# Performance work log

Measured on AMD Instinct MI355X. Metric: run time of the kernel, lower is better.

## Reference

```python
import jax, jax.numpy as jnp
import numpy as np


def setup_inputs() -> dict:
    key = jax.random.key(0)
    k0, k1, k2, k3 = jax.random.split(key, 4)
    B, in_dim, n_vars, out_dim, E = 64, 512, 512, 720, 8
    x = jax.random.normal(k0, (B, in_dim, n_vars), dtype=jnp.float32)
    # Gating: nn.Linear(in_dim, E, bias=False) -> weight [E, in_dim]
    Wg = jax.random.normal(k1, (E, in_dim), dtype=jnp.float32) * 0.02
    # Experts: nn.Linear(in_dim, out_dim) -> weight [out_dim, in_dim], bias [out_dim]
    We = jax.random.normal(k2, (E, out_dim, in_dim), dtype=jnp.float32) * 0.02
    be = jax.random.normal(k3, (E, out_dim), dtype=jnp.float32) * 0.02
    return {"x": x, "Wg": Wg, "We": We, "be": be, "top_k": 2}


def reference(x, Wg, We, be, top_k):
    # x: [B, in_len, n_vars] -> tokens along n_vars with feature dim in_len
    xt = jnp.swapaxes(x, 1, 2)                      # [B, V, D]
    gate = jax.nn.softmax(xt @ Wg.T, axis=-1)       # [B, V, E]
    weights, sel = jax.lax.top_k(gate, top_k)       # [B, V, k]
    E, O, D = We.shape
    out = jnp.zeros(xt.shape[:2] + (O,), dtype=xt.dtype)  # [B, V, O]
    for e in range(E):
        # combine weight for expert e: sum over top-k slots routed to e
        coef = jnp.sum(jnp.where(sel == e, weights, jnp.zeros_like(weights)), axis=-1)  # [B, V]
        out = out + coef[..., None] * (jnp.einsum('bvd,od->bvo', xt, We[e]) + be[e])
    return jnp.swapaxes(out, 1, 2)                  # [B, pred_len, n_vars]
```

## Files before the change

kernel.cpp:

```cpp
#include <hip/hip_runtime.h>
#include <hip/hip_bf16.h>

#define DID 512
#define NV  512
#define NB  64
#define OD  720
#define OPAD 768
#define NE  8
#define NTOK (NB * NV)
#define MAXTILE 512

typedef short  bf16x8 __attribute__((ext_vector_type(8)));
typedef float  f32x4  __attribute__((ext_vector_type(4)));

#define XT_OFF    0u
#define WB_OFF    33554432u
#define PID_OFF   39845888u
#define C1D_OFF   39976960u
#define C2D_OFF   40108032u
#define TL_OFF    40239104u
#define CL1_OFF   40370176u
#define CL2_OFF   40501248u
#define BCNT_OFF  40632320u
#define BFILL_OFF 40632576u
#define BOFF_OFF  40632832u
#define TPID_OFF  40633088u
#define TT0_OFF   40635136u
#define TEND_OFF  40637184u
#define NT_OFF    40639232u
#define SCR_OFF   40639488u
#define SCR_END   87825408u

static __device__ __forceinline__ ushort f2bf(float f) {
  unsigned u = __float_as_uint(f);
  unsigned r = (u + 0x7fffu + ((u >> 16) & 1u)) >> 16;
  return (ushort)r;
}
static __device__ __forceinline__ float bf2f(ushort u) {
  return __uint_as_float(((unsigned)u) << 16);
}
static __device__ __forceinline__ void async16(const ushort* g, ushort* l) {
  __builtin_amdgcn_global_load_lds((__attribute__((address_space(1))) void*)(g),
                                   (__attribute__((address_space(3))) void*)(l),
                                   16, 0, 0);
}
static __device__ __forceinline__ int swz(int r) { return (r & 3) ^ ((r >> 2) & 1); }

__global__ __launch_bounds__(512) void k_gatet(const float* __restrict__ x,
                                               const float* __restrict__ Wg,
                                               ushort* __restrict__ xt,
                                               int* __restrict__ pairid,
                                               float* __restrict__ c1d,
                                               float* __restrict__ c2d,
                                               int* __restrict__ bcnt) {
  __shared__ float wg[NE * DID];
  __shared__ float part[8][64][NE + 1];
  __shared__ int cnt64[64];
  const int tid = threadIdx.x;
  for (int i = tid; i < NE * DID / 4; i += 512)
    ((float4*)wg)[i] = ((const float4*)Wg)[i];
  if (tid < 64) cnt64[tid] = 0;
  __syncthreads();

  const int b    = blockIdx.y;
  const int v0   = blockIdx.x * 64;
  const int w    = tid >> 6;
  const int lane = tid & 63;
  const int v    = v0 + lane;
  const int d0   = w * 64;
  const float* xp = x + ((size_t)b * DID + d0) * NV + v;
  ushort* xtp = xt + ((size_t)b * NV + v) * DID + d0;

  float acc[NE];
#pragma unroll
  for (int e = 0; e < NE; ++e) acc[e] = 0.f;

  for (int c = 0; c < 64; c += 8) {
    float xv[8];
#pragma unroll
    for (int u = 0; u < 8; ++u) xv[u] = xp[(size_t)(c + u) * NV];
#pragma unroll
    for (int e = 0; e < NE; ++e) {
      const float* wp = &wg[e * DID + d0 + c];
      float4 wa = *(const float4*)wp;
      float4 wb4 = *(const float4*)(wp + 4);
      acc[e] += xv[0] * wa.x + xv[1] * wa.y + xv[2] * wa.z + xv[3] * wa.w
              + xv[4] * wb4.x + xv[5] * wb4.y + xv[6] * wb4.z + xv[7] * wb4.w;
    }
    bf16x8 pk;
#pragma unroll
    for (int u = 0; u < 8; ++u) pk[u] = (short)f2bf(xv[u]);
    *(bf16x8*)(xtp + c) = pk;
  }

#pragma unroll
  for (int e = 0; e < NE; ++e) part[w][lane][e] = acc[e];
  __syncthreads();

  if (tid < 64) {
    float a[NE];
#pragma unroll
    for (int e = 0; e < NE; ++e) {
      float s = part[0][tid][e];
#pragma unroll
      for (int q = 1; q < 8; ++q) s += part[q][tid][e];
      a[e] = s;
    }
    float mx = a[0];
#pragma unroll
    for (int e = 1; e < NE; ++e) mx = fmaxf(mx, a[e]);
    float sum = 0.f;
#pragma unroll
    for (int e = 0; e < NE; ++e) { a[e] = __expf(a[e] - mx); sum += a[e]; }
    const float inv = 1.f / sum;

    int i1 = 0; float g1 = a[0];
#pragma unroll
    for (int e = 1; e < NE; ++e) if (a[e] > g1) { g1 = a[e]; i1 = e; }
    int i2 = -1; float g2 = -1.f;
#pragma unroll
    for (int e = 0; e < NE; ++e) if (e != i1 && a[e] > g2) { g2 = a[e]; i2 = e; }
    g1 *= inv; g2 *= inv;

    int ea, eb; float ca, cb;
    if (i1 < i2) { ea = i1; eb = i2; ca = g1; cb = g2; }
    else         { ea = i2; eb = i1; ca = g2; cb = g1; }
    const int pid = ea * 8 + eb;
    const int t = b * NV + v0 + tid;
    pairid[t] = pid; c1d[t] = ca; c2d[t] = cb;
    atomicAdd(&cnt64[pid], 1);
  }
  __syncthreads();
  if (tid < 64 && cnt64[tid]) atomicAdd(&bcnt[tid], cnt64[tid]);
}

__global__ __launch_bounds__(256) void k_wbconv(const float* __restrict__ We,
                                                ushort* __restrict__ wb) {
  const int e = blockIdx.y;
  const int i = blockIdx.x * 256 + threadIdx.x;
  const int o = i >> 9;
  ushort val = 0;
  if (o < OD) val = f2bf(We[(size_t)e * OD * DID + i]);
  wb[(size_t)e * OPAD * DID + i] = val;
}

__global__ void k_prefix(const int* __restrict__ bcnt, int* __restrict__ boffs,
                         int* __restrict__ tpid, int* __restrict__ tt0,
                         int* __restrict__ tend, int* __restrict__ ntp) {
  const int p = threadIdx.x;
  const int c = bcnt[p];
  int run = c;
#pragma unroll
  for (int s = 1; s < 64; s <<= 1) {
    int up = __shfl_up(run, s, 64);
    if (p >= s) run += up;
  }
  const int excl = run - c;
  boffs[p] = excl;
  const int ntiles = (c + 127) >> 7;
  int trun = ntiles;
#pragma unroll
  for (int s = 1; s < 64; s <<= 1) {
    int up = __shfl_up(trun, s, 64);
    if (p >= s) trun += up;
  }
  const int texcl = trun - ntiles;
  for (int i = 0; i < ntiles; ++i) {
    tpid[texcl + i] = p;
    tt0[texcl + i]  = excl + i * 128;
    tend[texcl + i] = excl + c;
  }
  if (p == 63) ntp[0] = texcl + ntiles;
}

__global__ __launch_bounds__(256) void k_scatter(const int* __restrict__ pairid,
                                                 const float* __restrict__ c1d,
                                                 const float* __restrict__ c2d,
                                                 const int* __restrict__ boffs,
                                                 int* __restrict__ bfill,
                                                 int* __restrict__ tlist,
                                                 float* __restrict__ cl1,
                                                 float* __restrict__ cl2) {
  __shared__ int cnt64[64], base64[64];
  const int tid = threadIdx.x;
  if (tid < 64) cnt64[tid] = 0;
  __syncthreads();
  const int t = blockIdx.x * 256 + tid;
  const int pid = pairid[t];
  const int p = atomicAdd(&cnt64[pid], 1);
  __syncthreads();
  if (tid < 64) base64[tid] = cnt64[tid] ? atomicAdd(&bfill[tid], cnt64[tid]) : 0;
  __syncthreads();
  const int slot = boffs[pid] + base64[pid] + p;
  tlist[slot] = t; cl1[slot] = c1d[t]; cl2[slot] = c2d[t];
}

__global__ __launch_bounds__(256, 2) void k_gemm(
    const ushort* __restrict__ xt, const ushort* __restrict__ wb,
    const float* __restrict__ be, const int* __restrict__ tlist,
    const float* __restrict__ cl1, const float* __restrict__ cl2,
    const int* __restrict__ tpid, const int* __restrict__ tt0,
    const int* __restrict__ tendarr, const int* __restrict__ ntp,
    ushort* __restrict__ scratch, float* __restrict__ out, int mode) {
  const int tile = blockIdx.x;
  if (tile >= ntp[0]) return;
  const int pid  = tpid[tile];
  const int t0   = tt0[tile];
  const int tend = tendarr[tile];
  const int e1 = pid >> 3, e2 = pid & 7;
  const int o0 = blockIdx.y * 256;

  __shared__ __align__(16) ushort As[3][8192];
  __shared__ __align__(16) ushort Bs[3][4096];

  const int tid  = threadIdx.x;
  const int lane = tid & 63;
  const int w    = tid >> 6;

  int aoffA[4];
#pragma unroll
  for (int i = 0; i < 4; ++i) {
    const int f = w * 256 + i * 64 + lane;
    const int r = f >> 2, p = f & 3, q = p ^ swz(r);
    aoffA[i] = (o0 + r) * DID + q * 8;
  }
  int boffB[2];
#pragma unroll
  for (int i = 0; i < 2; ++i) {
    const int f = w * 128 + i * 64 + lane;
    const int r = f >> 2, p = f & 3, q = p ^ swz(r);
    const int sl = t0 + r;
    const int tk = (sl < tend) ? tlist[sl] : 0;
    boffB[i] = tk * DID + q * 8;
  }

  const int m    = lane & 15;
  const int quad = lane >> 4;
  const int wt   = (w & 1) * 64;
  const int wo   = (w >> 1) * 128;

  float ratio[4], c2v[4]; int tokv[4]; bool gv[4];
#pragma unroll
  for (int j = 0; j < 4; ++j) {
    const int sl = t0 + wt + j * 16 + m;
    gv[j] = sl < tend;
    const float cc1 = gv[j] ? cl1[sl] : 0.f;
    const float cc2 = gv[j] ? cl2[sl] : 1.f;
    ratio[j] = cc1 / cc2;
    c2v[j]   = gv[j] ? cc2 : 0.f;
    tokv[j]  = gv[j] ? tlist[sl] : 0;
  }

  f32x4 acc[8][4];
#pragma unroll
  for (int i = 0; i < 8; ++i)
#pragma unroll
    for (int j = 0; j < 4; ++j) acc[i][j] = (f32x4){0.f, 0.f, 0.f, 0.f};

#define STAGE(t, buf) do {                                          \
    const int eA_ = ((t) < 16) ? e1 : e2;                           \
    const int k0_ = ((t) & 15) * 32;                                \
    const ushort* wA_ = wb + (size_t)eA_ * OPAD * DID + k0_;        \
    async16(wA_ + aoffA[0], &As[buf][w * 2048]);                    \
    async16(wA_ + aoffA[1], &As[buf][w * 2048 + 512]);              \
    async16(wA_ + aoffA[2], &As[buf][w * 2048 + 1024]);             \
    async16(wA_ + aoffA[3], &As[buf][w * 2048 + 1536]);             \
    async16(xt + boffB[0] + k0_, &Bs[buf][w * 1024]);               \
    async16(xt + boffB[1] + k0_, &Bs[buf][w * 1024 + 512]);         \
  } while (0)

#define FRAGS(buf)                                                       \
    bf16x8 af[8], bfr[4];                                                \
    {                                                                    \
      const ushort* Asb = &As[buf][0];                                   \
      const ushort* Bsb = &Bs[buf][0];                                   \
      _Pragma("unroll")                                                  \
      for (int i = 0; i < 8; ++i) {                                      \
        const int R = wo + i * 16 + m;                                   \
        af[i] = *(const bf16x8*)(Asb + R * 32 + ((quad ^ swz(R)) << 3)); \
      }                                                                  \
      _Pragma("unroll")                                                  \
      for (int j = 0; j < 4; ++j) {                                      \
        const int R = wt + j * 16 + m;                                   \
        bfr[j] = *(const bf16x8*)(Bsb + R * 32 + ((quad ^ swz(R)) << 3));\
      }                                                                  \
    }

#define MFMA32()                                                         \
    __builtin_amdgcn_s_setprio(1);                                       \
    _Pragma("unroll")                                                    \
    for (int i = 0; i < 8; ++i)                                          \
      _Pragma("unroll")                                                  \
      for (int j = 0; j < 4; ++j)                                        \
        acc[i][j] = __builtin_amdgcn_mfma_f32_16x16x32_bf16(af[i], bfr[j],\
                                                            acc[i][j], 0, 0, 0); \
    __builtin_amdgcn_s_setprio(0);

  STAGE(0, 0);
  STAGE(1, 1);
  STAGE(2, 2);

  int cur = 0;
  for (int kk = 0; kk < 29; ++kk) {
    asm volatile("s_waitcnt vmcnt(12)" ::: "memory");
    __builtin_amdgcn_s_barrier();

    if (kk == 16) {
      const float* be1p = be + e1 * OD;
#pragma unroll
      for (int i = 0; i < 8; ++i) {
        const int ob = o0 + wo + i * 16 + quad * 4;
        float b0 = 0, b1 = 0, b2 = 0, b3 = 0;
        if (ob < OD) { b0 = be1p[ob]; b1 = be1p[ob + 1]; b2 = be1p[ob + 2]; b3 = be1p[ob + 3]; }
#pragma unroll
        for (int j = 0; j < 4; ++j) {
          acc[i][j][0] = (acc[i][j][0] + b0) * ratio[j];
          acc[i][j][1] = (acc[i][j][1] + b1) * ratio[j];
          acc[i][j][2] = (acc[i][j][2] + b2) * ratio[j];
          acc[i][j][3] = (acc[i][j][3] + b3) * ratio[j];
        }
      }
    }

    FRAGS(cur)
    asm volatile("s_waitcnt lgkmcnt(0)" ::: "memory");
    __builtin_amdgcn_s_barrier();
    STAGE(kk + 3, cur);
    MFMA32()
    cur = (cur == 2) ? 0 : cur + 1;
  }

  {
    asm volatile("s_waitcnt vmcnt(12)" ::: "memory");
    __builtin_amdgcn_s_barrier();
    FRAGS(2)
    MFMA32()
  }
  {
    asm volatile("s_waitcnt vmcnt(6)" ::: "memory");
    __builtin_amdgcn_s_barrier();
    FRAGS(0)
    MFMA32()
  }
  {
    asm volatile("s_waitcnt vmcnt(0)" ::: "memory");
    __builtin_amdgcn_s_barrier();
    FRAGS(1)
    MFMA32()
  }

#undef STAGE
#undef FRAGS
#undef MFMA32

  const float* be2p = be + e2 * OD;
#pragma unroll
  for (int i = 0; i < 8; ++i) {
    const int ob = o0 + wo + i * 16 + quad * 4;
    if (ob < OD) {
      const float b0 = be2p[ob], b1 = be2p[ob + 1], b2 = be2p[ob + 2], b3 = be2p[ob + 3];
#pragma unroll
      for (int j = 0; j < 4; ++j) {
        if (gv[j]) {
          const float v0 = c2v[j] * (acc[i][j][0] + b0);
          const float v1 = c2v[j] * (acc[i][j][1] + b1);
          const float v2 = c2v[j] * (acc[i][j][2] + b2);
          const float v3 = c2v[j] * (acc[i][j][3] + b3);
          if (mode == 0) {
            ushort4 pk = make_ushort4(f2bf(v0), f2bf(v1), f2bf(v2), f2bf(v3));
            *(ushort4*)(scratch + (size_t)tokv[j] * OD + ob) = pk;
          } else {
            const int bb = tokv[j] >> 9, vv = tokv[j] & 511;
            float* op = out + ((size_t)bb * OD + ob) * NV + vv;
            op[0] = v0; op[(size_t)NV] = v1; op[2 * (size_t)NV] = v2; op[3 * (size_t)NV] = v3;
          }
        }
      }
    }
  }
}

__global__ __launch_bounds__(256) void k_combine(const ushort* __restrict__ scratch,
                                                 float* __restrict__ out) {
  __shared__ ushort s[64][68];
  const int v0 = blockIdx.x * 64;
  const int o0 = blockIdx.y * 64;
  const int b  = blockIdx.z;
  const int tid = threadIdx.x;
#pragma unroll
  for (int it = 0; it < 2; ++it) {
    const int c = it * 256 + tid;
    const int row = c >> 3, cg = c & 7;
    const int o = o0 + cg * 8;
    if (o + 8 <= OD) {
      const ushort* src = scratch + ((size_t)(b * NV + v0 + row)) * OD + o;
      ushort4 ua = *(const ushort4*)(src);
      ushort4 ub = *(const ushort4*)(src + 4);
      *(ushort4*)&s[row][cg * 8] = ua;
      *(ushort4*)&s[row][cg * 8 + 4] = ub;
    }
  }
  __syncthreads();
  const int vv = tid & 63;
  const int og = tid >> 6;
#pragma unroll
  for (int oi = 0; oi < 8; ++oi) {
    const int ol = (og * 8 + oi) * 2;
    const int o = o0 + ol;
    if (o < OD) {
      ushort2 u = *(const ushort2*)&s[vv][ol];
      float* op = out + ((size_t)b * OD + o) * NV + v0 + vv;
      op[0]  = bf2f(u.x);
      op[NV] = bf2f(u.y);
    }
  }
}

extern "C" void kernel_launch(void* const* d_in, const int* in_sizes, int n_in,
                              void* d_out, int out_size, void* d_ws, size_t ws_size,
                              hipStream_t stream) {
  const float* x  = (const float*)d_in[0];
  const float* Wg = (const float*)d_in[1];
  const float* We = (const float*)d_in[2];
  const float* be = (const float*)d_in[3];
  float* out = (float*)d_out;

  char* ws = (char*)d_ws;
  ushort* xt     = (ushort*)(ws + XT_OFF);
  ushort* wb     = (ushort*)(ws + WB_OFF);
  int*    pairid = (int*)   (ws + PID_OFF);
  float*  c1d    = (float*) (ws + C1D_OFF);
  float*  c2d    = (float*) (ws + C2D_OFF);
  int*    tlist  = (int*)   (ws + TL_OFF);
  float*  cl1    = (float*) (ws + CL1_OFF);
  float*  cl2    = (float*) (ws + CL2_OFF);
  int*    bcnt   = (int*)   (ws + BCNT_OFF);
  int*    bfill  = (int*)   (ws + BFILL_OFF);
  int*    boffs  = (int*)   (ws + BOFF_OFF);
  int*    tpid   = (int*)   (ws + TPID_OFF);
  int*    tt0    = (int*)   (ws + TT0_OFF);
  int*    tend   = (int*)   (ws + TEND_OFF);
  int*    ntp    = (int*)   (ws + NT_OFF);
  ushort* scratch= (ushort*)(ws + SCR_OFF);

  const int mode = (ws_size >= (size_t)SCR_END) ? 0 : 1;

  (void)hipMemsetAsync(bcnt, 0, 512, stream);

  k_gatet<<<dim3(NV / 64, NB), 512, 0, stream>>>(x, Wg, xt, pairid, c1d, c2d, bcnt);
  k_wbconv<<<dim3(OPAD * DID / 256, NE), 256, 0, stream>>>(We, wb);
  k_prefix<<<1, 64, 0, stream>>>(bcnt, boffs, tpid, tt0, tend, ntp);
  k_scatter<<<NTOK / 256, 256, 0, stream>>>(pairid, c1d, c2d, boffs, bfill,
                                            tlist, cl1, cl2);
  k_gemm<<<dim3(320, OPAD / 256), 256, 0, stream>>>(xt, wb, be, tlist, cl1, cl2,
                                                    tpid, tt0, tend, ntp,
                                                    scratch, out, mode);
  if (mode == 0)
    k_combine<<<dim3(NV / 64, (OD + 63) / 64, NB), 256, 0, stream>>>(scratch, out);
}
```

Baseline: 307.6 us.

## Merge gating with weight conversion, fold prefix into scatter, restructure GEMM pipeline

The gating/transpose kernel and the expert-weight bf16 conversion now run as one launch, with extra blocks doing the conversion. The single-block prefix-scan kernel is removed: each scatter block recomputes the exclusive scan locally, and block 0 also writes the tile table. The GEMM main loop drops from a 3-deep to a 2-ahead prefetch with a single barrier per iteration, issuing the next stage before reading fragments. The aim is fewer launches and less per-iteration synchronisation. The cost is a shallower prefetch distance and redundant scan work in every scatter block.

After: 315.9 us. +2.7%, slower.

```diff
diff --git a/kernel.cpp b/kernel.cpp
--- a/kernel.cpp
+++ b/kernel.cpp
@@ -46,24 +46,39 @@
 }
 static __device__ __forceinline__ int swz(int r) { return (r & 3) ^ ((r >> 2) & 1); }
 
-__global__ __launch_bounds__(512) void k_gatet(const float* __restrict__ x,
-                                               const float* __restrict__ Wg,
-                                               ushort* __restrict__ xt,
-                                               int* __restrict__ pairid,
-                                               float* __restrict__ c1d,
-                                               float* __restrict__ c2d,
-                                               int* __restrict__ bcnt) {
+__global__ __launch_bounds__(512) void k_gatet_wb(const float* __restrict__ x,
+                                                  const float* __restrict__ Wg,
+                                                  const float* __restrict__ We,
+                                                  ushort* __restrict__ xt,
+                                                  ushort* __restrict__ wb,
+                                                  int* __restrict__ pairid,
+                                                  float* __restrict__ c1d,
+                                                  float* __restrict__ c2d,
+                                                  int* __restrict__ bcnt) {
+  const int bid = blockIdx.x;
+  const int tid = threadIdx.x;
+
+  if (bid >= 512) {
+    const int idx = (bid - 512) * 512 + tid;
+    const int e = idx / (OPAD * DID);
+    const int r = idx - e * (OPAD * DID);
+    const int o = r >> 9;
+    ushort val = 0;
+    if (o < OD) val = f2bf(We[(size_t)e * OD * DID + r]);
+    wb[(size_t)e * OPAD * DID + idx - e * (OPAD * DID)] = val;
+    return;
+  }
+
   __shared__ float wg[NE * DID];
   __shared__ float part[8][64][NE + 1];
   __shared__ int cnt64[64];
-  const int tid = threadIdx.x;
   for (int i = tid; i < NE * DID / 4; i += 512)
     ((float4*)wg)[i] = ((const float4*)Wg)[i];
   if (tid < 64) cnt64[tid] = 0;
   __syncthreads();
 
-  const int b    = blockIdx.y;
-  const int v0   = blockIdx.x * 64;
+  const int b    = bid >> 3;
+  const int v0   = (bid & 7) * 64;
   const int w    = tid >> 6;
   const int lane = tid & 63;
   const int v    = v0 + lane;
@@ -134,56 +149,48 @@
   if (tid < 64 && cnt64[tid]) atomicAdd(&bcnt[tid], cnt64[tid]);
 }
 
-__global__ __launch_bounds__(256) void k_wbconv(const float* __restrict__ We,
-                                                ushort* __restrict__ wb) {
-  const int e = blockIdx.y;
-  const int i = blockIdx.x * 256 + threadIdx.x;
-  const int o = i >> 9;
-  ushort val = 0;
-  if (o < OD) val = f2bf(We[(size_t)e * OD * DID + i]);
-  wb[(size_t)e * OPAD * DID + i] = val;
-}
-
-__global__ void k_prefix(const int* __restrict__ bcnt, int* __restrict__ boffs,
-                         int* __restrict__ tpid, int* __restrict__ tt0,
-                         int* __restrict__ tend, int* __restrict__ ntp) {
-  const int p = threadIdx.x;
-  const int c = bcnt[p];
-  int run = c;
-#pragma unroll
-  for (int s = 1; s < 64; s <<= 1) {
-    int up = __shfl_up(run, s, 64);
-    if (p >= s) run += up;
-  }
-  const int excl = run - c;
-  boffs[p] = excl;
-  const int ntiles = (c + 127) >> 7;
-  int trun = ntiles;
-#pragma unroll
-  for (int s = 1; s < 64; s <<= 1) {
-    int up = __shfl_up(trun, s, 64);
-    if (p >= s) trun += up;
-  }
-  const int texcl = trun - ntiles;
-  for (int i = 0; i < ntiles; ++i) {
-    tpid[texcl + i] = p;
-    tt0[texcl + i]  = excl + i * 128;
-    tend[texcl + i] = excl + c;
-  }
-  if (p == 63) ntp[0] = texcl + ntiles;
-}
-
 __global__ __launch_bounds__(256) void k_scatter(const int* __restrict__ pairid,
                                                  const float* __restrict__ c1d,
                                                  const float* __restrict__ c2d,
-                                                 const int* __restrict__ boffs,
+                                                 const int* __restrict__ bcnt,
                                                  int* __restrict__ bfill,
                                                  int* __restrict__ tlist,
                                                  float* __restrict__ cl1,
-                                                 float* __restrict__ cl2) {
-  __shared__ int cnt64[64], base64[64];
+                                                 float* __restrict__ cl2,
+                                                 int* __restrict__ tpid,
+                                                 int* __restrict__ tt0,
+                                                 int* __restrict__ tend,
+                                                 int* __restrict__ ntp) {
+  __shared__ int cnt64[64], base64[64], boffl[64];
   const int tid = threadIdx.x;
-  if (tid < 64) cnt64[tid] = 0;
+  if (tid < 64) {
+    const int c = bcnt[tid];
+    int run = c;
+#pragma unroll
+    for (int s = 1; s < 64; s <<= 1) {
+      int up = __shfl_up(run, s, 64);
+      if (tid >= s) run += up;
+    }
+    const int excl = run - c;
+    boffl[tid] = excl;
+    cnt64[tid] = 0;
+    if (blockIdx.x == 0) {
+      const int ntiles = (c + 127) >> 7;
+      int trun = ntiles;
+#pragma unroll
+      for (int s = 1; s < 64; s <<= 1) {
+        int up = __shfl_up(trun, s, 64);
+        if (tid >= s) trun += up;
+      }
+      const int texcl = trun - ntiles;
+      for (int i = 0; i < ntiles; ++i) {
+        tpid[texcl + i] = tid;
+        tt0[texcl + i]  = excl + i * 128;
+        tend[texcl + i] = run;
+      }
+      if (tid == 63) ntp[0] = trun;
+    }
+  }
   __syncthreads();
   const int t = blockIdx.x * 256 + tid;
   const int pid = pairid[t];
@@ -191,7 +198,7 @@
   __syncthreads();
   if (tid < 64) base64[tid] = cnt64[tid] ? atomicAdd(&bfill[tid], cnt64[tid]) : 0;
   __syncthreads();
-  const int slot = boffs[pid] + base64[pid] + p;
+  const int slot = boffl[pid] + base64[pid] + p;
   tlist[slot] = t; cl1[slot] = c1d[t]; cl2[slot] = c2d[t];
 }
 
@@ -298,13 +305,12 @@
 
   STAGE(0, 0);
   STAGE(1, 1);
-  STAGE(2, 2);
 
   int cur = 0;
-  for (int kk = 0; kk < 29; ++kk) {
-    asm volatile("s_waitcnt vmcnt(12)" ::: "memory");
+  int st  = 2;
+  for (int kk = 0; kk < 30; ++kk) {
+    asm volatile("s_waitcnt vmcnt(6)" ::: "memory");
     __builtin_amdgcn_s_barrier();
-
     if (kk == 16) {
       const float* be1p = be + e1 * OD;
 #pragma unroll
@@ -322,20 +328,13 @@
       }
     }
 
+    STAGE(kk + 2, st);
     FRAGS(cur)
-    asm volatile("s_waitcnt lgkmcnt(0)" ::: "memory");
-    __builtin_amdgcn_s_barrier();
-    STAGE(kk + 3, cur);
     MFMA32()
     cur = (cur == 2) ? 0 : cur + 1;
-  }
-
-  {
-    asm volatile("s_waitcnt vmcnt(12)" ::: "memory");
-    __builtin_amdgcn_s_barrier();
-    FRAGS(2)
-    MFMA32()
-  }
+    st  = (st  == 2) ? 0 : st  + 1;
+  }
+
   {
     asm volatile("s_waitcnt vmcnt(6)" ::: "memory");
     __builtin_amdgcn_s_barrier();
@@ -436,7 +435,6 @@
   float*  cl2    = (float*) (ws + CL2_OFF);
   int*    bcnt   = (int*)   (ws + BCNT_OFF);
   int*    bfill  = (int*)   (ws + BFILL_OFF);
-  int*    boffs  = (int*)   (ws + BOFF_OFF);
   int*    tpid   = (int*)   (ws + TPID_OFF);
   int*    tt0    = (int*)   (ws + TT0_OFF);
   int*    tend   = (int*)   (ws + TEND_OFF);
@@ -447,11 +445,11 @@
 
   (void)hipMemsetAsync(bcnt, 0, 512, stream);
 
-  k_gatet<<<dim3(NV / 64, NB), 512, 0, stream>>>(x, Wg, xt, pairid, c1d, c2d, bcnt);
-  k_wbconv<<<dim3(OPAD * DID / 256, NE), 256, 0, stream>>>(We, wb);
-  k_prefix<<<1, 64, 0, stream>>>(bcnt, boffs, tpid, tt0, tend, ntp);
-  k_scatter<<<NTOK / 256, 256, 0, stream>>>(pairid, c1d, c2d, boffs, bfill,
-                                            tlist, cl1, cl2);
+  k_gatet_wb<<<dim3(512 + NE * OPAD * DID / 512), 512, 0, stream>>>(
+      x, Wg, We, xt, wb, pairid, c1d, c2d, bcnt);
+  k_scatter<<<NTOK / 256, 256, 0, stream>>>(pairid, c1d, c2d, bcnt, bfill,
+                                            tlist, cl1, cl2,
+                                            tpid, tt0, tend, ntp);
   k_gemm<<<dim3(320, OPAD / 256), 256, 0, stream>>>(xt, wb, be, tlist, cl1, cl2,
                                                     tpid, tt0, tend, ntp,
                                                     scratch, out, mode);
```

## Stage transposed bf16 tile in LDS for coalesced writes; fold prefix into scatter

Applied to the files above, without the earlier changes.

The gate/transpose kernel now writes each token's bf16 row into a swizzled 64x512 LDS tile, then stores it to global memory in coalesced 16-byte chunks per row instead of strided per-thread writes. The LDS buffers are reused for the partial gate sums and the counters. Separately, the single-block prefix kernel is removed: each scatter block recomputes the 64-entry exclusive scan locally, and block 0 writes the tile lists. This saves one launch but adds two extra barriers and a large LDS footprint that may limit occupancy of the gate kernel.

After: 468.9 us. +52.4%, slower.

```diff
diff --git a/kernel.cpp b/kernel.cpp
--- a/kernel.cpp
+++ b/kernel.cpp
@@ -53,13 +53,14 @@
                                                float* __restrict__ c1d,
                                                float* __restrict__ c2d,
                                                int* __restrict__ bcnt) {
-  __shared__ float wg[NE * DID];
-  __shared__ float part[8][64][NE + 1];
-  __shared__ int cnt64[64];
+  __shared__ float  wg[NE * DID];
+  __shared__ ushort tile[64 * 512];
+  int*   cnt64 = (int*)wg;
+  float* partf = (float*)tile;
+
   const int tid = threadIdx.x;
   for (int i = tid; i < NE * DID / 4; i += 512)
     ((float4*)wg)[i] = ((const float4*)Wg)[i];
-  if (tid < 64) cnt64[tid] = 0;
   __syncthreads();
 
   const int b    = blockIdx.y;
@@ -69,12 +70,12 @@
   const int v    = v0 + lane;
   const int d0   = w * 64;
   const float* xp = x + ((size_t)b * DID + d0) * NV + v;
-  ushort* xtp = xt + ((size_t)b * NV + v) * DID + d0;
 
   float acc[NE];
 #pragma unroll
   for (int e = 0; e < NE; ++e) acc[e] = 0.f;
 
+  const int swl = lane & 7;
   for (int c = 0; c < 64; c += 8) {
     float xv[8];
 #pragma unroll
@@ -90,20 +91,35 @@
     bf16x8 pk;
 #pragma unroll
     for (int u = 0; u < 8; ++u) pk[u] = (short)f2bf(xv[u]);
-    *(bf16x8*)(xtp + c) = pk;
-  }
-
-#pragma unroll
-  for (int e = 0; e < NE; ++e) part[w][lane][e] = acc[e];
+    const int k = w * 8 + (c >> 3);
+    *(bf16x8*)&tile[lane * 512 + ((k ^ swl) << 3)] = pk;
+  }
+  __syncthreads();
+
+  if (tid < 64) cnt64[tid] = 0;
+
+  {
+    ushort* xtb = xt + ((size_t)b * NV + v0) * DID;
+#pragma unroll
+    for (int pass = 0; pass < 8; ++pass) {
+      const int vr = pass * 8 + w;
+      bf16x8 val = *(const bf16x8*)&tile[vr * 512 + ((lane ^ (vr & 7)) << 3)];
+      *(bf16x8*)(xtb + (size_t)vr * DID + lane * 8) = val;
+    }
+  }
+  __syncthreads();
+
+#pragma unroll
+  for (int e = 0; e < NE; ++e) partf[(w * 64 + lane) * 9 + e] = acc[e];
   __syncthreads();
 
   if (tid < 64) {
     float a[NE];
 #pragma unroll
     for (int e = 0; e < NE; ++e) {
-      float s = part[0][tid][e];
-#pragma unroll
-      for (int q = 1; q < 8; ++q) s += part[q][tid][e];
+      float s = partf[tid * 9 + e];
+#pragma unroll
+      for (int q = 1; q < 8; ++q) s += partf[(q * 64 + tid) * 9 + e];
       a[e] = s;
     }
     float mx = a[0];
@@ -144,46 +160,48 @@
   wb[(size_t)e * OPAD * DID + i] = val;
 }
 
-__global__ void k_prefix(const int* __restrict__ bcnt, int* __restrict__ boffs,
-                         int* __restrict__ tpid, int* __restrict__ tt0,
-                         int* __restrict__ tend, int* __restrict__ ntp) {
-  const int p = threadIdx.x;
-  const int c = bcnt[p];
-  int run = c;
-#pragma unroll
-  for (int s = 1; s < 64; s <<= 1) {
-    int up = __shfl_up(run, s, 64);
-    if (p >= s) run += up;
-  }
-  const int excl = run - c;
-  boffs[p] = excl;
-  const int ntiles = (c + 127) >> 7;
-  int trun = ntiles;
-#pragma unroll
-  for (int s = 1; s < 64; s <<= 1) {
-    int up = __shfl_up(trun, s, 64);
-    if (p >= s) trun += up;
-  }
-  const int texcl = trun - ntiles;
-  for (int i = 0; i < ntiles; ++i) {
-    tpid[texcl + i] = p;
-    tt0[texcl + i]  = excl + i * 128;
-    tend[texcl + i] = excl + c;
-  }
-  if (p == 63) ntp[0] = texcl + ntiles;
-}
-
 __global__ __launch_bounds__(256) void k_scatter(const int* __restrict__ pairid,
                                                  const float* __restrict__ c1d,
                                                  const float* __restrict__ c2d,
-                                                 const int* __restrict__ boffs,
+                                                 const int* __restrict__ bcnt,
                                                  int* __restrict__ bfill,
                                                  int* __restrict__ tlist,
                                                  float* __restrict__ cl1,
-                                                 float* __restrict__ cl2) {
-  __shared__ int cnt64[64], base64[64];
+                                                 float* __restrict__ cl2,
+                                                 int* __restrict__ tpid,
+                                                 int* __restrict__ tt0,
+                                                 int* __restrict__ tend,
+                                                 int* __restrict__ ntp) {
+  __shared__ int cnt64[64], base64[64], boffl[64];
   const int tid = threadIdx.x;
-  if (tid < 64) cnt64[tid] = 0;
+  if (tid < 64) {
+    const int c = bcnt[tid];
+    int run = c;
+#pragma unroll
+    for (int s = 1; s < 64; s <<= 1) {
+      int up = __shfl_up(run, s, 64);
+      if (tid >= s) run += up;
+    }
+    const int excl = run - c;
+    boffl[tid] = excl;
+    cnt64[tid] = 0;
+    if (blockIdx.x == 0) {
+      const int ntiles = (c + 127) >> 7;
+      int trun = ntiles;
+#pragma unroll
+      for (int s = 1; s < 64; s <<= 1) {
+        int up = __shfl_up(trun, s, 64);
+        if (tid >= s) trun += up;
+      }
+      const int texcl = trun - ntiles;
+      for (int i = 0; i < ntiles; ++i) {
+        tpid[texcl + i] = tid;
+        tt0[texcl + i]  = excl + i * 128;
+        tend[texcl + i] = run;
+      }
+      if (tid == 63) ntp[0] = trun;
+    }
+  }
   __syncthreads();
   const int t = blockIdx.x * 256 + tid;
   const int pid = pairid[t];
@@ -191,7 +209,7 @@
   __syncthreads();
   if (tid < 64) base64[tid] = cnt64[tid] ? atomicAdd(&bfill[tid], cnt64[tid]) : 0;
   __syncthreads();
-  const int slot = boffs[pid] + base64[pid] + p;
+  const int slot = boffl[pid] + base64[pid] + p;
   tlist[slot] = t; cl1[slot] = c1d[t]; cl2[slot] = c2d[t];
 }
 
@@ -436,7 +454,6 @@
   float*  cl2    = (float*) (ws + CL2_OFF);
   int*    bcnt   = (int*)   (ws + BCNT_OFF);
   int*    bfill  = (int*)   (ws + BFILL_OFF);
-  int*    boffs  = (int*)   (ws + BOFF_OFF);
   int*    tpid   = (int*)   (ws + TPID_OFF);
   int*    tt0    = (int*)   (ws + TT0_OFF);
   int*    tend   = (int*)   (ws + TEND_OFF);
@@ -449,9 +466,9 @@
 
   k_gatet<<<dim3(NV / 64, NB), 512, 0, stream>>>(x, Wg, xt, pairid, c1d, c2d, bcnt);
   k_wbconv<<<dim3(OPAD * DID / 256, NE), 256, 0, stream>>>(We, wb);
-  k_prefix<<<1, 64, 0, stream>>>(bcnt, boffs, tpid, tt0, tend, ntp);
-  k_scatter<<<NTOK / 256, 256, 0, stream>>>(pairid, c1d, c2d, boffs, bfill,
-                                            tlist, cl1, cl2);
+  k_scatter<<<NTOK / 256, 256, 0, stream>>>(pairid, c1d, c2d, bcnt, bfill,
+                                            tlist, cl1, cl2,
+                                            tpid, tt0, tend, ntp);
   k_gemm<<<dim3(320, OPAD / 256), 256, 0, stream>>>(xt, wb, be, tlist, cl1, cl2,
                                                     tpid, tt0, tend, ntp,
                                                     scratch, out, mode);
```
